# Optimization experiments

Measured on AMD Instinct MI355X. Metric: run time of the kernel, lower is better.

The kernel has to match this reference:

```python
import jax, jax.numpy as jnp
import numpy as np

HEADS = 20
NUM_AOE = 16
NUM_IP = 16


def setup_inputs() -> dict:
    key = jax.random.key(0)
    ks = jax.random.split(key, 7)
    B, Sq, H = 8, 4096, 1280
    Skv, C = 109, 768
    scale = 0.02
    return {
        "hidden_states": jax.random.normal(ks[0], (B, Sq, H), jnp.float32),
        "encoder_hidden_states": jax.random.normal(ks[1], (B, Skv, C), jnp.float32),
        "Wq": jax.random.normal(ks[2], (H, H), jnp.float32) * scale,
        "Wk": jax.random.normal(ks[3], (C, H), jnp.float32) * scale,
        "Wv": jax.random.normal(ks[4], (C, H), jnp.float32) * scale,
        "Wo": jax.random.normal(ks[5], (H, H), jnp.float32) * scale,
        "bo": jnp.zeros((H,), jnp.float32),
    }


def reference(hidden_states, encoder_hidden_states, Wq, Wk, Wv, Wo, bo):
    B, Sq, H = hidden_states.shape
    Skv = encoder_hidden_states.shape[1]
    head_dim = H // HEADS
    residual = hidden_states

    # projections (no bias on q/k/v, as in diffusers SD attention)
    q = (hidden_states @ Wq).reshape(B, Sq, HEADS, head_dim).transpose(0, 2, 1, 3)
    k = (encoder_hidden_states @ Wk).reshape(B, Skv, HEADS, head_dim).transpose(0, 2, 1, 3)
    v = (encoder_hidden_states @ Wv).reshape(B, Skv, HEADS, head_dim).transpose(0, 2, 1, 3)

    # manual attention: QK^T / sqrt(d), softmax
    scores = jnp.einsum("bhqd,bhkd->bhqk", q, k) / jnp.sqrt(jnp.asarray(head_dim, q.dtype))
    probs = jax.nn.softmax(scores, axis=-1)

    # frequency_mode != 'both': rescale aoe (first NUM_AOE) and image (last NUM_IP)
    # key-token ranges post-softmax, then renormalize. scale_aoe = scale_ip = 1
    # in this config, but the renormalization math is kept faithfully.
    scale_aoe = jnp.asarray(1.0, probs.dtype)
    scale_ip = jnp.asarray(1.0, probs.dtype)
    idx = jnp.arange(Skv)
    scale_vector = jnp.where(idx < NUM_AOE, scale_aoe, 1.0)
    scale_vector = jnp.where(idx >= Skv - NUM_IP, scale_vector * scale_ip, scale_vector)
    probs = probs * scale_vector  # broadcasts over (B, HEADS, Sq, Skv)
    probs = probs / probs.sum(axis=-1, keepdims=True)

    out = jnp.einsum("bhqk,bhkd->bhqd", probs, v)
    out = out.transpose(0, 2, 1, 3).reshape(B, Sq, H)
    out = out @ Wo + bo
    # residual connection, rescale_output_factor = 1.0
    return out + residual
```

## Files before the change

### kernel.cpp

```cpp
#include <hip/hip_runtime.h>
#include <hip/hip_bf16.h>

typedef unsigned short u16;
typedef __attribute__((ext_vector_type(8))) short short8;
typedef __attribute__((ext_vector_type(4))) short short4v;
typedef __attribute__((ext_vector_type(4))) float f32x4;

#define HEADS 20
#define HD 64
#define BB 8
#define SQ 4096
#define HDIM 1280
#define SKV 109
#define CDIM 768
#define SKV_PAD 128
#define SKV_T 112

#define SBAR() asm volatile("s_barrier" ::: "memory")

static __device__ __forceinline__ u16 f2bf(float x) {
  union { __hip_bfloat16 h; u16 u; } cv;
  cv.h = __float2bfloat16(x);
  return cv.u;
}

static __device__ __forceinline__ void gll16(const void* g, void* l) {
  __builtin_amdgcn_global_load_lds(
      (const __attribute__((address_space(1))) unsigned int*)g,
      (__attribute__((address_space(3))) unsigned int*)l, 16, 0, 0);
}

__global__ __launch_bounds__(256) void prep_all(
    const float* __restrict__ Wq, const float* __restrict__ Wk,
    const float* __restrict__ Wv, const float* __restrict__ Wo,
    const float* __restrict__ ehs, u16* __restrict__ wqt,
    u16* __restrict__ wkt, u16* __restrict__ wvt, u16* __restrict__ wot,
    u16* __restrict__ ehsp) {
  const int id = blockIdx.x;
  if (id < 5120) {
    const float* W;
    u16* out;
    int K;
    float scale;
    int base;
    if (id < 1600) {
      W = Wq; out = wqt; K = HDIM; scale = 0.125f; base = 0;
    } else if (id < 2560) {
      W = Wk; out = wkt; K = CDIM; scale = 1.0f; base = 1600;
    } else if (id < 3520) {
      W = Wv; out = wvt; K = CDIM; scale = 1.0f; base = 2560;
    } else {
      W = Wo; out = wot; K = HDIM; scale = 1.0f; base = 3520;
    }
    const int lid = id - base;
    const int bx = lid % 40, by = lid / 40;
    __shared__ float t[32][33];
    int tx = threadIdx.x & 31, ty = threadIdx.x >> 5;
    int n0 = bx * 32, k0 = by * 32;
#pragma unroll
    for (int i = 0; i < 32; i += 8)
      t[ty + i][tx] = W[(size_t)(k0 + ty + i) * HDIM + n0 + tx];
    __syncthreads();
#pragma unroll
    for (int i = 0; i < 32; i += 8)
      out[(size_t)(n0 + ty + i) * K + k0 + tx] = f2bf(t[tx][ty + i] * scale);
  } else {
    int idx = (id - 5120) * 256 + threadIdx.x;
    if (idx >= BB * SKV_PAD * CDIM / 4) return;
    int c4 = idx * 4;
    int b = c4 / (SKV_PAD * CDIM);
    int rem = c4 - b * (SKV_PAD * CDIM);
    int s = rem / CDIM;
    int c = rem - s * CDIM;
    short4v o = {0, 0, 0, 0};
    if (s < SKV) {
      f32x4 v = *(const f32x4*)(ehs + ((size_t)b * SKV + s) * CDIM + c);
#pragma unroll
      for (int j = 0; j < 4; j++) o[j] = (short)f2bf(v[j]);
    }
    *(short4v*)&ehsp[c4] = o;
  }
}

template <int MODE>
__global__ __launch_bounds__(512, 4)
void gemm_v2(const u16* __restrict__ A, const u16* __restrict__ Bt,
             void* __restrict__ outp, int K, int ntn,
             const float* __restrict__ bias, const float* __restrict__ resid) {
  __shared__ u16 lds[3][12288];
  const int tid = threadIdx.x;
  const int wid = tid >> 6, lane = tid & 63;
  const int wm = wid >> 2, wn = wid & 3;
  const int g = lane >> 4, r = lane & 15;

  const int nwg = gridDim.x;
  const int orig = blockIdx.x;
  const int wg = (orig & 7) * (nwg >> 3) + (orig >> 3);
  const int mt = wg / ntn, nt = wg - mt * ntn;
  const int row0 = mt * 128, col0 = nt * 256;

  const u16* Ag = A + (size_t)row0 * K;
  const u16* Bg = Bt + (size_t)col0 * K;
  const int NT = K >> 5;

  const int cx = (g * 8) ^ (((r >> 1) & 3) << 3);

  const int sa_row = tid >> 2;
  const int sa_sc = (tid & 3) ^ ((tid >> 3) & 3);
  const int sb_row1 = (tid + 512) >> 2;
  const int sb_sc1 = ((tid + 512) & 3) ^ (((tid + 512) >> 3) & 3);

  f32x4 acc[4][4] = {};

  auto stage = [&](int buf, int kt) {
    gll16(Ag + (size_t)sa_row * K + kt + sa_sc * 8, &lds[buf][tid * 8]);
    gll16(Bg + (size_t)sa_row * K + kt + sa_sc * 8, &lds[buf][4096 + tid * 8]);
    gll16(Bg + (size_t)sb_row1 * K + kt + sb_sc1 * 8,
          &lds[buf][4096 + (tid + 512) * 8]);
  };

  stage(0, 0);
  stage(1, 32);
  asm volatile("s_waitcnt vmcnt(3)" ::: "memory");
  SBAR();

  int buf = 0;
  for (int t = 0; t < NT; ++t) {
    int nb = buf + 2;
    if (nb >= 3) nb -= 3;
    if (t + 2 < NT) stage(nb, (t + 2) * 32);

    short8 a[4], b[4];
#pragma unroll
    for (int mi = 0; mi < 4; ++mi)
      a[mi] = *(short8*)&lds[buf][(wm * 64 + mi * 16 + r) * 32 + cx];
#pragma unroll
    for (int nf = 0; nf < 4; ++nf)
      b[nf] = *(short8*)&lds[buf][4096 + (wn * 64 + nf * 16 + r) * 32 + cx];

    __builtin_amdgcn_s_setprio(1);
#pragma unroll
    for (int mi = 0; mi < 4; ++mi)
#pragma unroll
      for (int nf = 0; nf < 4; ++nf)
        acc[mi][nf] = __builtin_amdgcn_mfma_f32_16x16x32_bf16(a[mi], b[nf],
                                                              acc[mi][nf], 0, 0, 0);
    __builtin_amdgcn_s_setprio(0);

    if (t < NT - 2)
      asm volatile("s_waitcnt vmcnt(3)" ::: "memory");
    else
      asm volatile("s_waitcnt vmcnt(0)" ::: "memory");
    SBAR();
    buf = (buf + 1 == 3) ? 0 : buf + 1;
  }

  if constexpr (MODE == 0) {
    u16* O = (u16*)outp;
#pragma unroll
    for (int mi = 0; mi < 4; ++mi)
#pragma unroll
      for (int i = 0; i < 4; ++i) {
        size_t m = row0 + wm * 64 + mi * 16 + g * 4 + i;
        size_t base = m * HDIM + col0 + wn * 64 + r;
#pragma unroll
        for (int nf = 0; nf < 4; ++nf)
          O[base + nf * 16] = f2bf(acc[mi][nf][i]);
      }
  } else {
    float* O = (float*)outp;
#pragma unroll
    for (int mi = 0; mi < 4; ++mi)
#pragma unroll
      for (int i = 0; i < 4; ++i) {
        size_t m = row0 + wm * 64 + mi * 16 + g * 4 + i;
        size_t base = m * HDIM + col0 + wn * 64 + r;
#pragma unroll
        for (int nf = 0; nf < 4; ++nf) {
          int col = col0 + wn * 64 + nf * 16 + r;
          O[base + nf * 16] = acc[mi][nf][i] + bias[col] + resid[base + nf * 16];
        }
      }
  }
}

__global__ __launch_bounds__(256, 4)
void gemm_kv_hs(const u16* __restrict__ A, const u16* __restrict__ Kt,
                const u16* __restrict__ Vt, u16* __restrict__ khb,
                u16* __restrict__ vtb, const float* __restrict__ hs,
                u16* __restrict__ hsb) {
  if (blockIdx.x >= 160) {
    const size_t total = (size_t)BB * SQ * HDIM;
    const int nb = gridDim.x - 160;
    size_t step = (size_t)nb * 256 * 8;
    for (size_t i = ((size_t)(blockIdx.x - 160) * 256 + threadIdx.x) * 8;
         i < total; i += step) {
      f32x4 a = *(const f32x4*)(hs + i);
      f32x4 b = *(const f32x4*)(hs + i + 4);
      short8 o;
#pragma unroll
      for (int j = 0; j < 4; j++) {
        o[j] = (short)f2bf(a[j]);
        o[j + 4] = (short)f2bf(b[j]);
      }
      *(short8*)&hsb[i] = o;
    }
    return;
  }

  __shared__ u16 Alds[128 * 32];
  __shared__ u16 Blds[128 * 32];
  const int tid = threadIdx.x;
  const int wid = tid >> 6, lane = tid & 63;
  const int wm = wid >> 1, wn = wid & 1;
  const int g = lane >> 4, r = lane & 15;

  const int half = blockIdx.x >= 80 ? 1 : 0;
  const u16* Bt = half ? Vt : Kt;
  const int orig = blockIdx.x - half * 80;
  const int wg = (orig & 7) * 10 + (orig >> 3);
  const int mt = wg / 10, nt = wg - mt * 10;
  const int row0 = mt * 128, col0 = nt * 128;
  const int erow = tid >> 2, ecol = (tid & 3) * 8;
  const int K = CDIM;

  f32x4 acc[4][4] = {};

  for (int kt = 0; kt < K; kt += 32) {
    const u16* ag = A + (size_t)(row0 + erow) * K + kt + ecol;
    const u16* bg = Bt + (size_t)(col0 + erow) * K + kt + ecol;
    gll16(ag, &Alds[erow * 32 + ecol]);
    gll16(ag + (size_t)64 * K, &Alds[(erow + 64) * 32 + ecol]);
    gll16(bg, &Blds[erow * 32 + ecol]);
    gll16(bg + (size_t)64 * K, &Blds[(erow + 64) * 32 + ecol]);
    __syncthreads();

    short8 afr[4], bfr[4];
#pragma unroll
    for (int mi = 0; mi < 4; mi++)
      afr[mi] = *(short8*)&Alds[(wm * 64 + mi * 16 + r) * 32 + g * 8];
#pragma unroll
    for (int ni = 0; ni < 4; ni++)
      bfr[ni] = *(short8*)&Blds[(wn * 64 + ni * 16 + r) * 32 + g * 8];
#pragma unroll
    for (int mi = 0; mi < 4; mi++)
#pragma unroll
      for (int ni = 0; ni < 4; ni++)
        acc[mi][ni] = __builtin_amdgcn_mfma_f32_16x16x32_bf16(afr[mi], bfr[ni],
                                                              acc[mi][ni], 0, 0, 0);
    __syncthreads();
  }

  u16* O = half ? vtb : khb;
#pragma unroll
  for (int mi = 0; mi < 4; mi++)
#pragma unroll
    for (int i = 0; i < 4; i++) {
      int m = row0 + wm * 64 + mi * 16 + g * 4 + i;
      int b = m >> 7, skv = m & 127;
#pragma unroll
      for (int ni = 0; ni < 4; ni++) {
        int col = col0 + wn * 64 + ni * 16 + r;
        int hh = col >> 6, d = col & 63;
        size_t addr;
        if (half)
          addr = (((size_t)b * HEADS + hh) * HD + d) * SKV_PAD + skv;
        else
          addr = (((size_t)b * HEADS + hh) * SKV_PAD + skv) * HD + d;
        O[addr] = f2bf(acc[mi][ni][i]);
      }
    }
}

__global__ __launch_bounds__(256, 2)
void attn_kernel(const u16* __restrict__ q, const u16* __restrict__ kh,
                 const u16* __restrict__ vt, u16* __restrict__ o) {
  __shared__ u16 Klds[SKV_T * 72];
  __shared__ u16 Vlds[HD * 136];
  __shared__ u16 Plds[4 * 16 * 136];
  __shared__ u16 Olds[4 * 16 * 72];
  const int tid = threadIdx.x;
  const int wid = tid >> 6, lane = tid & 63;
  const int g = lane >> 4, r = lane & 15;
  const int bh = blockIdx.y;
  const int b = bh / HEADS, h = bh - b * HEADS;
  const int qt0 = blockIdx.x * 8;

  const u16* kg = kh + (size_t)bh * SKV_PAD * HD;
  for (int i = tid; i < SKV_T * 8; i += 256) {
    int row = i >> 3, c = (i & 7) * 8;
    *(short8*)&Klds[row * 72 + c] = *(const short8*)(kg + row * HD + c);
  }
  const u16* vg = vt + (size_t)bh * HD * SKV_PAD;
  for (int i = tid; i < HD * 16; i += 256) {
    int row = i >> 4, c = (i & 15) * 8;
    *(short8*)&Vlds[row * 136 + c] = *(const short8*)(vg + row * SKV_PAD + c);
  }
  {
    short4v z = {0, 0, 0, 0};
    *(short4v*)&Plds[(wid * 16 + r) * 136 + 112 + g * 4] = z;
  }
  __syncthreads();

  const u16* qbase = q + ((size_t)b * SQ + wid * 16 + r) * HDIM + h * HD + g * 8;
  short8 aq0 = *(const short8*)(qbase + (size_t)qt0 * 64 * HDIM);
  short8 aq1 = *(const short8*)(qbase + (size_t)qt0 * 64 * HDIM + 32);

#pragma unroll 1
  for (int qs = 0; qs < 8; ++qs) {
    const int qt = qt0 + qs;

    f32x4 s[7];
#pragma unroll
    for (int nf = 0; nf < 7; nf++) {
      f32x4 z = {0.f, 0.f, 0.f, 0.f};
      short8 k0 = *(short8*)&Klds[(nf * 16 + r) * 72 + g * 8];
      short8 k1 = *(short8*)&Klds[(nf * 16 + r) * 72 + 32 + g * 8];
      z = __builtin_amdgcn_mfma_f32_16x16x32_bf16(aq0, k0, z, 0, 0, 0);
      z = __builtin_amdgcn_mfma_f32_16x16x32_bf16(aq1, k1, z, 0, 0, 0);
      s[nf] = z;
    }

    if (qs + 1 < 8) {
      aq0 = *(const short8*)(qbase + (size_t)(qt + 1) * 64 * HDIM);
      aq1 = *(const short8*)(qbase + (size_t)(qt + 1) * 64 * HDIM + 32);
    }

#pragma unroll
    for (int i = 0; i < 4; i++) {
      float pv[7];
      float mx = -1e30f;
#pragma unroll
      for (int nf = 0; nf < 7; nf++) {
        float v = s[nf][i];
        if (nf == 6 && r >= 13) v = -1e30f;
        pv[nf] = v;
        mx = fmaxf(mx, v);
      }
#pragma unroll
      for (int d = 1; d < 16; d <<= 1) mx = fmaxf(mx, __shfl_xor(mx, d, 64));
      float sum = 0.f;
#pragma unroll
      for (int nf = 0; nf < 7; nf++) {
        float e = (nf == 6 && r >= 13) ? 0.f : __expf(pv[nf] - mx);
        pv[nf] = e;
        sum += e;
      }
#pragma unroll
      for (int d = 1; d < 16; d <<= 1) sum += __shfl_xor(sum, d, 64);
      float is = 1.f / sum;
#pragma unroll
      for (int nf = 0; nf < 7; nf++)
        Plds[(wid * 16 + g * 4 + i) * 136 + nf * 16 + r] = f2bf(pv[nf] * is);
    }

    f32x4 oacc[4] = {};
#pragma unroll
    for (int kk = 0; kk < 4; kk++) {
      short8 ap = *(short8*)&Plds[(wid * 16 + r) * 136 + kk * 32 + g * 8];
#pragma unroll
      for (int nf = 0; nf < 4; nf++) {
        short8 bv = *(short8*)&Vlds[(nf * 16 + r) * 136 + kk * 32 + g * 8];
        oacc[nf] = __builtin_amdgcn_mfma_f32_16x16x32_bf16(ap, bv, oacc[nf], 0, 0, 0);
      }
    }

    u16* st = &Olds[wid * 16 * 72];
#pragma unroll
    for (int nf = 0; nf < 4; nf++)
#pragma unroll
      for (int i = 0; i < 4; i++)
        st[(g * 4 + i) * 72 + nf * 16 + r] = f2bf(oacc[nf][i]);
    u16* og = o + ((size_t)b * SQ + qt * 64 + wid * 16) * HDIM + h * HD;
#pragma unroll
    for (int j = 0; j < 2; ++j) {
      int chunk = lane + j * 64;
      int row = chunk >> 3, cc = (chunk & 7) * 8;
      *(short8*)&og[(size_t)row * HDIM + cc] = *(short8*)&st[row * 72 + cc];
    }
  }
}

extern "C" void kernel_launch(void* const* d_in, const int* in_sizes, int n_in,
                              void* d_out, int out_size, void* d_ws, size_t ws_size,
                              hipStream_t stream) {
  const float* hs  = (const float*)d_in[0];
  const float* ehs = (const float*)d_in[1];
  const float* Wq  = (const float*)d_in[2];
  const float* Wk  = (const float*)d_in[3];
  const float* Wv  = (const float*)d_in[4];
  const float* Wo  = (const float*)d_in[5];
  const float* bo  = (const float*)d_in[6];

  char* ws = (char*)d_ws;
  size_t off = 0;
  auto alloc = [&](size_t elems) {
    u16* p = (u16*)(ws + off);
    off += ((elems * 2 + 255) / 256) * 256;
    return p;
  };
  u16* wqt  = alloc((size_t)HDIM * HDIM);
  u16* wot  = alloc((size_t)HDIM * HDIM);
  u16* wkt  = alloc((size_t)HDIM * CDIM);
  u16* wvt  = alloc((size_t)HDIM * CDIM);
  u16* ehsp = alloc((size_t)BB * SKV_PAD * CDIM);
  u16* khb  = alloc((size_t)BB * HEADS * SKV_PAD * HD);
  u16* vtb  = alloc((size_t)BB * HEADS * HD * SKV_PAD);
  u16* qb   = alloc((size_t)BB * SQ * HDIM);
  u16* ao   = alloc((size_t)BB * SQ * HDIM);
  u16* hsb  = ao;

  prep_all<<<dim3(5888), 256, 0, stream>>>(Wq, Wk, Wv, Wo, ehs, wqt, wkt, wvt,
                                           wot, ehsp);
  gemm_kv_hs<<<dim3(2048), 256, 0, stream>>>(ehsp, wkt, wvt, khb, vtb, hs, hsb);
  gemm_v2<0><<<dim3(1280), 512, 0, stream>>>(hsb, wqt, qb, HDIM, 5, nullptr, nullptr);
  attn_kernel<<<dim3(SQ / 512, BB * HEADS), 256, 0, stream>>>(qb, khb, vtb, ao);
  gemm_v2<3><<<dim3(1280), 512, 0, stream>>>(ao, wot, (void*)d_out, HDIM, 5, bo, hs);
}
```

Measured before the change: 399.1 us.

## Fuse fp32-to-bf16 conversion of hidden states into the Q projection GEMM

Adds a Q-projection GEMM that reads fp32 hidden states straight from global memory into registers and converts them to bf16 just before the MFMA. This removes the separate conversion pass and the bf16 copy of hidden states. B is staged in LDS through a triple-buffered pipeline with 128x128 tiles. In exchange, each A element is read once per N-tile in fp32 (twice the bytes), the A tile is not shared through LDS, and conversion work is added to the inner loop. The KV GEMM kernel no longer does the conversion.

```diff
diff --git a/kernel.cpp b/kernel.cpp
--- a/kernel.cpp
+++ b/kernel.cpp
@@ -82,6 +82,101 @@
   }
 }
 
+__global__ __launch_bounds__(512, 4)
+void gemm_qf(const float* __restrict__ A, const u16* __restrict__ Bt,
+             u16* __restrict__ O) {
+  __shared__ u16 Bf[3][4096];
+  const int tid = threadIdx.x;
+  const int wid = tid >> 6, lane = tid & 63;
+  const int wm = wid >> 2, wn = wid & 3;
+  const int g = lane >> 4, r = lane & 15;
+
+  const int x = blockIdx.x & 7, l = blockIdx.x >> 3;
+  const int q = l / 10, nt = l - q * 10;
+  const int mt = x * 32 + q;
+  const int row0 = mt * 128, col0 = nt * 128;
+  const int K = HDIM;
+  const int NT = K >> 5;
+
+  const float* Ag = A + (size_t)(row0 + wm * 64 + r) * K + g * 8;
+  const u16* Bg = Bt + (size_t)col0 * K;
+
+  const int b_row = tid >> 2;
+  const int b_sc = (tid & 3) ^ ((b_row >> 1) & 3);
+
+  f32x4 acc[4][2] = {};
+  f32x4 vaE[4][2], vaO[4][2];
+
+  auto stageB = [&](int buf, int kt) {
+    gll16(Bg + (size_t)b_row * K + kt + b_sc * 8, &Bf[buf][tid * 8]);
+  };
+  auto loadA = [&](f32x4(&va)[4][2], int kt) {
+#pragma unroll
+    for (int mi = 0; mi < 4; ++mi) {
+      const float* p = Ag + (size_t)(mi * 16) * K + kt;
+      va[mi][0] = *(const f32x4*)p;
+      va[mi][1] = *(const f32x4*)(p + 4);
+    }
+  };
+
+  stageB(0, 0);
+  loadA(vaE, 0);
+  stageB(1, 32);
+
+  auto body = [&](f32x4(&cur)[4][2], f32x4(&nxt)[4][2], int t, int buf) {
+    if (t < NT - 2)
+      asm volatile("s_waitcnt vmcnt(1)" ::: "memory");
+    else
+      asm volatile("s_waitcnt vmcnt(0)" ::: "memory");
+    SBAR();
+    short8 a[4];
+#pragma unroll
+    for (int mi = 0; mi < 4; ++mi)
+#pragma unroll
+      for (int j = 0; j < 4; ++j) {
+        a[mi][j] = (short)f2bf(cur[mi][0][j]);
+        a[mi][j + 4] = (short)f2bf(cur[mi][1][j]);
+      }
+    short8 b[2];
+#pragma unroll
+    for (int nf = 0; nf < 2; ++nf) {
+      int row = wn * 32 + nf * 16 + r;
+      b[nf] = *(short8*)&Bf[buf][(row * 4 + (g ^ ((row >> 1) & 3))) * 8];
+    }
+    if (t + 1 < NT) loadA(nxt, (t + 1) * 32);
+    int nb = buf + 2;
+    if (nb >= 3) nb -= 3;
+    if (t + 2 < NT) stageB(nb, (t + 2) * 32);
+    __builtin_amdgcn_s_setprio(1);
+#pragma unroll
+    for (int mi = 0; mi < 4; ++mi)
+#pragma unroll
+      for (int nf = 0; nf < 2; ++nf)
+        acc[mi][nf] = __builtin_amdgcn_mfma_f32_16x16x32_bf16(a[mi], b[nf],
+                                                              acc[mi][nf], 0, 0, 0);
+    __builtin_amdgcn_s_setprio(0);
+  };
+
+  int buf = 0;
+  for (int t = 0; t < NT; t += 2) {
+    body(vaE, vaO, t, buf);
+    buf = (buf + 1 == 3) ? 0 : buf + 1;
+    body(vaO, vaE, t + 1, buf);
+    buf = (buf + 1 == 3) ? 0 : buf + 1;
+  }
+
+#pragma unroll
+  for (int mi = 0; mi < 4; ++mi)
+#pragma unroll
+    for (int i = 0; i < 4; ++i) {
+      size_t m = row0 + wm * 64 + mi * 16 + g * 4 + i;
+      size_t base = m * HDIM + col0 + wn * 32 + r;
+#pragma unroll
+      for (int nf = 0; nf < 2; ++nf)
+        O[base + nf * 16] = f2bf(acc[mi][nf][i]);
+    }
+}
+
 template <int MODE>
 __global__ __launch_bounds__(512, 4)
 void gemm_v2(const u16* __restrict__ A, const u16* __restrict__ Bt,
@@ -185,29 +280,9 @@
 }
 
 __global__ __launch_bounds__(256, 4)
-void gemm_kv_hs(const u16* __restrict__ A, const u16* __restrict__ Kt,
-                const u16* __restrict__ Vt, u16* __restrict__ khb,
-                u16* __restrict__ vtb, const float* __restrict__ hs,
-                u16* __restrict__ hsb) {
-  if (blockIdx.x >= 160) {
-    const size_t total = (size_t)BB * SQ * HDIM;
-    const int nb = gridDim.x - 160;
-    size_t step = (size_t)nb * 256 * 8;
-    for (size_t i = ((size_t)(blockIdx.x - 160) * 256 + threadIdx.x) * 8;
-         i < total; i += step) {
-      f32x4 a = *(const f32x4*)(hs + i);
-      f32x4 b = *(const f32x4*)(hs + i + 4);
-      short8 o;
-#pragma unroll
-      for (int j = 0; j < 4; j++) {
-        o[j] = (short)f2bf(a[j]);
-        o[j + 4] = (short)f2bf(b[j]);
-      }
-      *(short8*)&hsb[i] = o;
-    }
-    return;
-  }
-
+void gemm_kv(const u16* __restrict__ A, const u16* __restrict__ Kt,
+             const u16* __restrict__ Vt, u16* __restrict__ khb,
+             u16* __restrict__ vtb) {
   __shared__ u16 Alds[128 * 32];
   __shared__ u16 Blds[128 * 32];
   const int tid = threadIdx.x;
@@ -408,12 +483,11 @@
   u16* vtb  = alloc((size_t)BB * HEADS * HD * SKV_PAD);
   u16* qb   = alloc((size_t)BB * SQ * HDIM);
   u16* ao   = alloc((size_t)BB * SQ * HDIM);
-  u16* hsb  = ao;
 
   prep_all<<<dim3(5888), 256, 0, stream>>>(Wq, Wk, Wv, Wo, ehs, wqt, wkt, wvt,
                                            wot, ehsp);
-  gemm_kv_hs<<<dim3(2048), 256, 0, stream>>>(ehsp, wkt, wvt, khb, vtb, hs, hsb);
-  gemm_v2<0><<<dim3(1280), 512, 0, stream>>>(hsb, wqt, qb, HDIM, 5, nullptr, nullptr);
+  gemm_kv<<<dim3(160), 256, 0, stream>>>(ehsp, wkt, wvt, khb, vtb);
+  gemm_qf<<<dim3(2560), 512, 0, stream>>>(hs, wqt, qb);
   attn_kernel<<<dim3(SQ / 512, BB * HEADS), 256, 0, stream>>>(qb, khb, vtb, ao);
   gemm_v2<3><<<dim3(1280), 512, 0, stream>>>(ao, wot, (void*)d_out, HDIM, 5, bo, hs);
 }
```

Measured after the change: 1.188 ms. 2.98x slower.
